# Kernel tuning notes

Hardware: AMD Instinct MI355X
Metric: run time of the kernel (lower is better)

## Reference

```python
import jax, jax.numpy as jnp
import numpy as np

N_NODES = 50000
N_EDGES = 800000
F_IN = 128
F_HID = 128
N_CLS = 1
E_TR = 100000
E_TE = 20000


def setup_inputs() -> dict:
    key = jax.random.key(0)
    ks = jax.random.split(key, 16)
    inp = {
        'x': jax.random.normal(ks[0], (N_NODES, F_IN), dtype=jnp.float32),
        'edge_index': jax.random.randint(ks[1], (2, N_EDGES), 0, N_NODES, dtype=jnp.int32),
        'pos_edges_train': jax.random.randint(ks[2], (2, E_TR), 0, N_NODES, dtype=jnp.int32),
        'neg_edges_train': jax.random.randint(ks[3], (2, E_TR), 0, N_NODES, dtype=jnp.int32),
        'pos_edges_test': jax.random.randint(ks[4], (2, E_TE), 0, N_NODES, dtype=jnp.int32),
        'neg_edges_test': jax.random.randint(ks[5], (2, E_TE), 0, N_NODES, dtype=jnp.int32),
    }
    s = 0.05
    inp['W0'] = jax.random.normal(ks[6], (F_IN, F_HID), dtype=jnp.float32) * s
    inp['b0'] = jnp.zeros((F_HID,), dtype=jnp.float32)
    inp['W1'] = jax.random.normal(ks[7], (F_HID, F_HID), dtype=jnp.float32) * s
    inp['b1'] = jnp.zeros((F_HID,), dtype=jnp.float32)
    inp['W2'] = jax.random.normal(ks[8], (F_HID, F_HID), dtype=jnp.float32) * s
    inp['b2'] = jnp.zeros((F_HID,), dtype=jnp.float32)
    inp['W3'] = jax.random.normal(ks[9], (F_HID, F_HID), dtype=jnp.float32) * s
    inp['b3'] = jnp.zeros((F_HID,), dtype=jnp.float32)
    inp['Wl1'] = jax.random.normal(ks[10], (2 * F_HID, F_HID), dtype=jnp.float32) * s
    inp['bl1'] = jnp.zeros((F_HID,), dtype=jnp.float32)
    inp['Wl2'] = jax.random.normal(ks[11], (F_HID, N_CLS), dtype=jnp.float32) * s
    inp['bl2'] = jnp.zeros((N_CLS,), dtype=jnp.float32)
    return inp


def _gcn_conv(h, W, b, src, dst, dis):
    # PyG GCNConv: out = D^{-1/2}(A+I)D^{-1/2} (h W) + b, with self loops folded in analytically
    hw = h @ W                                           # [N, F]
    msg = hw[src] * dis[src][:, None]                    # [E, F]
    agg = jax.ops.segment_sum(msg, dst, num_segments=N_NODES)
    return agg * dis[:, None] + hw * (dis ** 2)[:, None] + b


def _edge_feats(x, e):
    return jnp.concatenate([x[e[0]], x[e[1]]], axis=1)


def reference(x, edge_index, pos_edges_train, neg_edges_train, pos_edges_test, neg_edges_test,
              W0, b0, W1, b1, W2, b2, W3, b3, Wl1, bl1, Wl2, bl2):
    src, dst = edge_index[0], edge_index[1]
    # degree with self loop (+1), symmetric normalization
    deg = jax.ops.segment_sum(jnp.ones((src.shape[0],), jnp.float32), dst, num_segments=N_NODES) + 1.0
    dis = deg ** -0.5

    h = jax.nn.relu(_gcn_conv(x, W0, b0, src, dst, dis))
    h = jax.nn.relu(_gcn_conv(h, W1, b1, src, dst, dis))
    h = jax.nn.relu(_gcn_conv(h, W2, b2, src, dst, dis))
    h = _gcn_conv(h, W3, b3, src, dst, dis)

    x_train = jnp.concatenate([_edge_feats(h, pos_edges_train), _edge_feats(h, neg_edges_train)], axis=0)
    x_test = jnp.concatenate([_edge_feats(h, pos_edges_test), _edge_feats(h, neg_edges_test)], axis=0)
    n_train = x_train.shape[0]
    z = jnp.concatenate([x_train, x_test], axis=0)
    z = jax.nn.relu(z @ Wl1 + bl1)
    z = (z @ Wl2 + bl2).squeeze(1)
    return (z[:n_train], z[n_train:])
```

## Files before the change

kernel.cpp:

```cpp
#include <hip/hip_runtime.h>
#include <math.h>

#define NN 50000
#define NE 800000
#define FD 128
#define SCAN_B 196
#define NTR 100000
#define NTE 20000


__global__ __launch_bounds__(256) void k_zero_int(int* __restrict__ p, int n) {
    int i = blockIdx.x * 256 + threadIdx.x;
    if (i < n) p[i] = 0;
}

__global__ __launch_bounds__(256) void k_count(const int* __restrict__ dst, int* __restrict__ deg) {
    int e = blockIdx.x * 256 + threadIdx.x;
    if (e < NE) atomicAdd(&deg[dst[e]], 1);
}


__global__ __launch_bounds__(256) void k_scan1(const int* __restrict__ deg,
                                               int* __restrict__ partial,
                                               int* __restrict__ bsum,
                                               float* __restrict__ dis) {
    __shared__ int wsum[4];
    const int t = threadIdx.x, lane = t & 63, wid = t >> 6;
    const int i = blockIdx.x * 256 + t;
    int v = (i < NN) ? deg[i] : 0;
    int sc = v;
#pragma unroll
    for (int d = 1; d < 64; d <<= 1) {
        int o = __shfl_up(sc, d, 64);
        if (lane >= d) sc += o;
    }
    if (lane == 63) wsum[wid] = sc;
    __syncthreads();
    int pre = 0;
    for (int w = 0; w < wid; ++w) pre += wsum[w];
    if (i < NN) {
        partial[i] = pre + sc - v;
        dis[i] = (float)(1.0 / sqrt((double)(v + 1)));
    }
    if (t == 255) bsum[blockIdx.x] = pre + sc;
}

__global__ __launch_bounds__(256) void k_scan2(int* __restrict__ bsum) {
    __shared__ int wsum[4];
    const int t = threadIdx.x, lane = t & 63, wid = t >> 6;
    int v = (t < SCAN_B) ? bsum[t] : 0;
    int sc = v;
#pragma unroll
    for (int d = 1; d < 64; d <<= 1) {
        int o = __shfl_up(sc, d, 64);
        if (lane >= d) sc += o;
    }
    if (lane == 63) wsum[wid] = sc;
    __syncthreads();
    int pre = 0;
    for (int w = 0; w < wid; ++w) pre += wsum[w];
    if (t < SCAN_B) bsum[t] = pre + sc - v;
}

__global__ __launch_bounds__(256) void k_scan3(const int* __restrict__ partial,
                                               const int* __restrict__ bsum,
                                               int* __restrict__ offs,
                                               int* __restrict__ cursor) {
    const int i = blockIdx.x * 256 + threadIdx.x;
    if (i < NN) {
        int o = partial[i] + bsum[blockIdx.x];
        offs[i] = o;
        cursor[i] = o;
    }
    if (i == 0) offs[NN] = NE;
}


__global__ __launch_bounds__(256) void k_fill(const int* __restrict__ src, const int* __restrict__ dst,
                                              int* __restrict__ cursor, int* __restrict__ srcs_sorted) {
    int e = blockIdx.x * 256 + threadIdx.x;
    if (e < NE) {
        int d = dst[e];
        int p = atomicAdd(&cursor[d], 1);
        srcs_sorted[p] = src[e];
    }
}


__global__ __launch_bounds__(256) void k_gemm(const float* __restrict__ A,
                                              const float* __restrict__ W,
                                              const float* __restrict__ dis,
                                              float* __restrict__ C, int nrows) {
    __shared__ float As[64][128];
    const int t = threadIdx.x;
    const int row0 = blockIdx.x * 64;

    for (int idx = t; idx < 64 * 32; idx += 256) {
        int r = idx >> 5, c = idx & 31;
        float4 v = make_float4(0.f, 0.f, 0.f, 0.f);
        if (row0 + r < nrows)
            v = reinterpret_cast<const float4*>(A)[(size_t)(row0 + r) * 32 + c];
        reinterpret_cast<float4*>(&As[r][0])[c] = v;
    }
    __syncthreads();

    const int cg = t & 31;
    const int eg = t >> 5;
    float acc[8][4] = {{0.f}};

    const float4* W4 = reinterpret_cast<const float4*>(W);
    const float4* As4 = reinterpret_cast<const float4*>(As);

    for (int k4 = 0; k4 < 32; ++k4) {
        float4 w0 = W4[(k4 * 4 + 0) * 32 + cg];
        float4 w1 = W4[(k4 * 4 + 1) * 32 + cg];
        float4 w2 = W4[(k4 * 4 + 2) * 32 + cg];
        float4 w3 = W4[(k4 * 4 + 3) * 32 + cg];
#pragma unroll
        for (int i = 0; i < 8; ++i) {
            float4 a = As4[(eg * 8 + i) * 32 + k4];
            acc[i][0] += a.x * w0.x + a.y * w1.x + a.z * w2.x + a.w * w3.x;
            acc[i][1] += a.x * w0.y + a.y * w1.y + a.z * w2.y + a.w * w3.y;
            acc[i][2] += a.x * w0.z + a.y * w1.z + a.z * w2.z + a.w * w3.z;
            acc[i][3] += a.x * w0.w + a.y * w1.w + a.z * w2.w + a.w * w3.w;
        }
    }

#pragma unroll
    for (int i = 0; i < 8; ++i) {
        int r = row0 + eg * 8 + i;
        if (r < nrows) {
            float d = dis[r];
            float4 o = make_float4(acc[i][0] * d, acc[i][1] * d, acc[i][2] * d, acc[i][3] * d);
            reinterpret_cast<float4*>(C)[(size_t)r * 32 + cg] = o;
        }
    }
}


__global__ __launch_bounds__(256) void k_gemm_uv(const float* __restrict__ A,
                                                 const float* __restrict__ Wa,
                                                 const float* __restrict__ Wb,
                                                 float* __restrict__ U,
                                                 float* __restrict__ V, int nrows) {
    __shared__ float As[64][128];
    const int t = threadIdx.x;
    const int row0 = blockIdx.x * 64;

    for (int idx = t; idx < 64 * 32; idx += 256) {
        int r = idx >> 5, c = idx & 31;
        float4 v = make_float4(0.f, 0.f, 0.f, 0.f);
        if (row0 + r < nrows)
            v = reinterpret_cast<const float4*>(A)[(size_t)(row0 + r) * 32 + c];
        reinterpret_cast<float4*>(&As[r][0])[c] = v;
    }
    __syncthreads();

    const int cg = t & 31;
    const int eg = t >> 5;
    float accU[8][4] = {{0.f}};
    float accV[8][4] = {{0.f}};

    const float4* Wa4 = reinterpret_cast<const float4*>(Wa);
    const float4* Wb4 = reinterpret_cast<const float4*>(Wb);
    const float4* As4 = reinterpret_cast<const float4*>(As);

    for (int k = 0; k < 128; k += 2) {
        float4 wa0 = Wa4[(k + 0) * 32 + cg];
        float4 wa1 = Wa4[(k + 1) * 32 + cg];
        float4 wb0 = Wb4[(k + 0) * 32 + cg];
        float4 wb1 = Wb4[(k + 1) * 32 + cg];
#pragma unroll
        for (int i = 0; i < 8; ++i) {
            float2 a = reinterpret_cast<const float2*>(&As[eg * 8 + i][0])[k >> 1];
            accU[i][0] += a.x * wa0.x + a.y * wa1.x;
            accU[i][1] += a.x * wa0.y + a.y * wa1.y;
            accU[i][2] += a.x * wa0.z + a.y * wa1.z;
            accU[i][3] += a.x * wa0.w + a.y * wa1.w;
            accV[i][0] += a.x * wb0.x + a.y * wb1.x;
            accV[i][1] += a.x * wb0.y + a.y * wb1.y;
            accV[i][2] += a.x * wb0.z + a.y * wb1.z;
            accV[i][3] += a.x * wb0.w + a.y * wb1.w;
        }
    }

#pragma unroll
    for (int i = 0; i < 8; ++i) {
        int r = row0 + eg * 8 + i;
        if (r < nrows) {
            reinterpret_cast<float4*>(U)[(size_t)r * 32 + cg] =
                make_float4(accU[i][0], accU[i][1], accU[i][2], accU[i][3]);
            reinterpret_cast<float4*>(V)[(size_t)r * 32 + cg] =
                make_float4(accV[i][0], accV[i][1], accV[i][2], accV[i][3]);
        }
    }
}


template <bool RELU>
__global__ __launch_bounds__(256) void k_gather(const float* __restrict__ hws,
                                                const float* __restrict__ dis,
                                                const float* __restrict__ b,
                                                const int* __restrict__ offs,
                                                const int* __restrict__ srcs,
                                                float* __restrict__ out) {
    const int t = threadIdx.x;
    const int slice = blockIdx.x & 7;
    const int node = (blockIdx.x >> 3) * 64 + (t >> 2);
    if (node >= NN) return;
    const int f4 = slice * 4 + (t & 3);

    const float4* H4 = reinterpret_cast<const float4*>(hws);
    float4 acc = H4[(size_t)node * 32 + f4];
    const int e0 = offs[node], e1 = offs[node + 1];
    int e = e0;
    for (; e + 4 <= e1; e += 4) {
        int s0 = srcs[e + 0], s1 = srcs[e + 1], s2 = srcs[e + 2], s3 = srcs[e + 3];
        float4 v0 = H4[(size_t)s0 * 32 + f4];
        float4 v1 = H4[(size_t)s1 * 32 + f4];
        float4 v2 = H4[(size_t)s2 * 32 + f4];
        float4 v3 = H4[(size_t)s3 * 32 + f4];
        acc.x += v0.x + v1.x + v2.x + v3.x;
        acc.y += v0.y + v1.y + v2.y + v3.y;
        acc.z += v0.z + v1.z + v2.z + v3.z;
        acc.w += v0.w + v1.w + v2.w + v3.w;
    }
    for (; e < e1; ++e) {
        int s = srcs[e];
        float4 v = H4[(size_t)s * 32 + f4];
        acc.x += v.x; acc.y += v.y; acc.z += v.z; acc.w += v.w;
    }
    float d = dis[node];
    float4 bb = reinterpret_cast<const float4*>(b)[f4];
    float4 o;
    o.x = acc.x * d + bb.x;
    o.y = acc.y * d + bb.y;
    o.z = acc.z * d + bb.z;
    o.w = acc.w * d + bb.w;
    if (RELU) {
        o.x = fmaxf(o.x, 0.f); o.y = fmaxf(o.y, 0.f);
        o.z = fmaxf(o.z, 0.f); o.w = fmaxf(o.w, 0.f);
    }
    reinterpret_cast<float4*>(out)[(size_t)node * 32 + f4] = o;
}


__global__ __launch_bounds__(256) void k_edge_score(const float* __restrict__ U,
                                                    const float* __restrict__ V,
                                                    const int* __restrict__ tp,
                                                    const int* __restrict__ tn,
                                                    const int* __restrict__ sp,
                                                    const int* __restrict__ sn,
                                                    const float* __restrict__ bl1,
                                                    const float* __restrict__ Wl2,
                                                    const float* __restrict__ bl2,
                                                    float* __restrict__ out) {
    const int t = threadIdx.x;
    const int f4 = t & 31;
    const int e = blockIdx.x * 8 + (t >> 5);
    if (e >= 2 * NTR + 2 * NTE) return;

    int a, bn;
    if (e < NTR)                { a = tp[e];              bn = tp[e + NTR]; }
    else if (e < 2 * NTR)       { a = tn[e - NTR];        bn = tn[e]; }
    else if (e < 2 * NTR + NTE) { a = sp[e - 2 * NTR];    bn = sp[e - 2 * NTR + NTE]; }
    else                        { a = sn[e - 2 * NTR - NTE]; bn = sn[e - 2 * NTR]; }

    float4 u = reinterpret_cast<const float4*>(U)[(size_t)a * 32 + f4];
    float4 v = reinterpret_cast<const float4*>(V)[(size_t)bn * 32 + f4];
    float4 bb = reinterpret_cast<const float4*>(bl1)[f4];
    float4 w2 = reinterpret_cast<const float4*>(Wl2)[f4];

    float s = fmaxf(u.x + v.x + bb.x, 0.f) * w2.x
            + fmaxf(u.y + v.y + bb.y, 0.f) * w2.y
            + fmaxf(u.z + v.z + bb.z, 0.f) * w2.z
            + fmaxf(u.w + v.w + bb.w, 0.f) * w2.w;
#pragma unroll
    for (int m = 16; m >= 1; m >>= 1) s += __shfl_xor(s, m, 64);
    if (f4 == 0) out[e] = s + bl2[0];
}


extern "C" void kernel_launch(void* const* d_in, const int* in_sizes, int n_in,
                              void* d_out, int out_size, void* d_ws, size_t ws_size,
                              hipStream_t stream) {
    const float* x = (const float*)d_in[0];
    const int* ei = (const int*)d_in[1];
    const int* srcp = ei;
    const int* dstp = ei + NE;

    const int* e_tr_pos = (const int*)d_in[2];
    const int* e_tr_neg = (const int*)d_in[3];
    const int* e_te_pos = (const int*)d_in[4];
    const int* e_te_neg = (const int*)d_in[5];

    const float* W[4] = {(const float*)d_in[6], (const float*)d_in[8],
                         (const float*)d_in[10], (const float*)d_in[12]};
    const float* b[4] = {(const float*)d_in[7], (const float*)d_in[9],
                         (const float*)d_in[11], (const float*)d_in[13]};
    const float* Wl1 = (const float*)d_in[14];
    const float* bl1 = (const float*)d_in[15];
    const float* Wl2 = (const float*)d_in[16];
    const float* bl2 = (const float*)d_in[17];

    float* ws = (float*)d_ws;
    float* dis = ws;
    int* deg = (int*)(ws + 50176);
    int* offs = (int*)(ws + 100352);
    int* cursor = (int*)(ws + 150784);
    int* bsum = (int*)(ws + 200960);
    int* srcs = (int*)(ws + 201216);
    float* B0 = ws + 1001216;
    float* B1 = B0 + 6400000;
    float* B2 = B1 + 6400000;
    int* partial = (int*)B2;

    k_zero_int<<<(NN + 255) / 256, 256, 0, stream>>>(deg, NN);
    k_count<<<(NE + 255) / 256, 256, 0, stream>>>(dstp, deg);
    k_scan1<<<SCAN_B, 256, 0, stream>>>(deg, partial, bsum, dis);
    k_scan2<<<1, 256, 0, stream>>>(bsum);
    k_scan3<<<SCAN_B, 256, 0, stream>>>(partial, bsum, offs, cursor);
    k_fill<<<(NE + 255) / 256, 256, 0, stream>>>(srcp, dstp, cursor, srcs);

    const int gemm_blocks = (NN + 63) / 64;
    const int gath_blocks = ((NN + 63) / 64) * 8;

    float* hout[4] = {B1, B2, B1, B2};
    const float* hin = x;
    for (int l = 0; l < 4; ++l) {
        k_gemm<<<gemm_blocks, 256, 0, stream>>>(hin, W[l], dis, B0, NN);
        if (l < 3)
            k_gather<true><<<gath_blocks, 256, 0, stream>>>(B0, dis, b[l], offs, srcs, hout[l]);
        else
            k_gather<false><<<gath_blocks, 256, 0, stream>>>(B0, dis, b[l], offs, srcs, hout[l]);
        hin = hout[l];
    }

    const float* hfin = B2;
    float* Ubuf = B0;
    float* Vbuf = B1;
    k_gemm_uv<<<gemm_blocks, 256, 0, stream>>>(hfin, Wl1, Wl1 + 128 * 128, Ubuf, Vbuf, NN);

    float* out = (float*)d_out;
    const int n_all = 2 * NTR + 2 * NTE;
    k_edge_score<<<(n_all + 7) / 8, 256, 0, stream>>>(Ubuf, Vbuf,
                                                      e_tr_pos, e_tr_neg, e_te_pos, e_te_neg,
                                                      bl1, Wl2, bl2, out);
}
```

Before: 653.9 us.

## Remap gather to one node per 32 lanes, unroll by 8, prefetch GEMM weights

The gather kernel now assigns 32 lanes per node covering all 128 features in one block instead of splitting features into 8 block slices, so each neighbor row is read as one contiguous 512-byte access. Its edge loop is unrolled to 8 loads with a tree reduction to raise memory-level parallelism. The GEMM kernel software-prefetches the next weight slice into registers, and the UV GEMM switches to float4 LDS reads with a 4-wide k step. These changes target gather latency and load efficiency at the cost of more registers per thread.

```diff
diff --git a/kernel.cpp b/kernel.cpp
--- a/kernel.cpp
+++ b/kernel.cpp
@@ -111,11 +111,17 @@
     const float4* W4 = reinterpret_cast<const float4*>(W);
     const float4* As4 = reinterpret_cast<const float4*>(As);
 
+    float4 w0 = W4[0 * 32 + cg];
+    float4 w1 = W4[1 * 32 + cg];
+    float4 w2 = W4[2 * 32 + cg];
+    float4 w3 = W4[3 * 32 + cg];
+
     for (int k4 = 0; k4 < 32; ++k4) {
-        float4 w0 = W4[(k4 * 4 + 0) * 32 + cg];
-        float4 w1 = W4[(k4 * 4 + 1) * 32 + cg];
-        float4 w2 = W4[(k4 * 4 + 2) * 32 + cg];
-        float4 w3 = W4[(k4 * 4 + 3) * 32 + cg];
+        int kn = (k4 < 31) ? (k4 + 1) : 31;
+        float4 n0 = W4[(kn * 4 + 0) * 32 + cg];
+        float4 n1 = W4[(kn * 4 + 1) * 32 + cg];
+        float4 n2 = W4[(kn * 4 + 2) * 32 + cg];
+        float4 n3 = W4[(kn * 4 + 3) * 32 + cg];
 #pragma unroll
         for (int i = 0; i < 8; ++i) {
             float4 a = As4[(eg * 8 + i) * 32 + k4];
@@ -124,6 +130,7 @@
             acc[i][2] += a.x * w0.z + a.y * w1.z + a.z * w2.z + a.w * w3.z;
             acc[i][3] += a.x * w0.w + a.y * w1.w + a.z * w2.w + a.w * w3.w;
         }
+        w0 = n0; w1 = n1; w2 = n2; w3 = n3;
     }
 
 #pragma unroll
@@ -165,22 +172,26 @@
     const float4* Wb4 = reinterpret_cast<const float4*>(Wb);
     const float4* As4 = reinterpret_cast<const float4*>(As);
 
-    for (int k = 0; k < 128; k += 2) {
-        float4 wa0 = Wa4[(k + 0) * 32 + cg];
-        float4 wa1 = Wa4[(k + 1) * 32 + cg];
-        float4 wb0 = Wb4[(k + 0) * 32 + cg];
-        float4 wb1 = Wb4[(k + 1) * 32 + cg];
+    for (int k4 = 0; k4 < 32; ++k4) {
+        float4 wa0 = Wa4[(k4 * 4 + 0) * 32 + cg];
+        float4 wa1 = Wa4[(k4 * 4 + 1) * 32 + cg];
+        float4 wa2 = Wa4[(k4 * 4 + 2) * 32 + cg];
+        float4 wa3 = Wa4[(k4 * 4 + 3) * 32 + cg];
+        float4 wb0 = Wb4[(k4 * 4 + 0) * 32 + cg];
+        float4 wb1 = Wb4[(k4 * 4 + 1) * 32 + cg];
+        float4 wb2 = Wb4[(k4 * 4 + 2) * 32 + cg];
+        float4 wb3 = Wb4[(k4 * 4 + 3) * 32 + cg];
 #pragma unroll
         for (int i = 0; i < 8; ++i) {
-            float2 a = reinterpret_cast<const float2*>(&As[eg * 8 + i][0])[k >> 1];
-            accU[i][0] += a.x * wa0.x + a.y * wa1.x;
-            accU[i][1] += a.x * wa0.y + a.y * wa1.y;
-            accU[i][2] += a.x * wa0.z + a.y * wa1.z;
-            accU[i][3] += a.x * wa0.w + a.y * wa1.w;
-            accV[i][0] += a.x * wb0.x + a.y * wb1.x;
-            accV[i][1] += a.x * wb0.y + a.y * wb1.y;
-            accV[i][2] += a.x * wb0.z + a.y * wb1.z;
-            accV[i][3] += a.x * wb0.w + a.y * wb1.w;
+            float4 a = As4[(eg * 8 + i) * 32 + k4];
+            accU[i][0] += a.x * wa0.x + a.y * wa1.x + a.z * wa2.x + a.w * wa3.x;
+            accU[i][1] += a.x * wa0.y + a.y * wa1.y + a.z * wa2.y + a.w * wa3.y;
+            accU[i][2] += a.x * wa0.z + a.y * wa1.z + a.z * wa2.z + a.w * wa3.z;
+            accU[i][3] += a.x * wa0.w + a.y * wa1.w + a.z * wa2.w + a.w * wa3.w;
+            accV[i][0] += a.x * wb0.x + a.y * wb1.x + a.z * wb2.x + a.w * wb3.x;
+            accV[i][1] += a.x * wb0.y + a.y * wb1.y + a.z * wb2.y + a.w * wb3.y;
+            accV[i][2] += a.x * wb0.z + a.y * wb1.z + a.z * wb2.z + a.w * wb3.z;
+            accV[i][3] += a.x * wb0.w + a.y * wb1.w + a.z * wb2.w + a.w * wb3.w;
         }
     }
 
@@ -205,25 +216,29 @@
                                                 const int* __restrict__ srcs,
                                                 float* __restrict__ out) {
     const int t = threadIdx.x;
-    const int slice = blockIdx.x & 7;
-    const int node = (blockIdx.x >> 3) * 64 + (t >> 2);
+    const int f4 = t & 31;
+    const int node = blockIdx.x * 8 + (t >> 5);
     if (node >= NN) return;
-    const int f4 = slice * 4 + (t & 3);
 
     const float4* H4 = reinterpret_cast<const float4*>(hws);
     float4 acc = H4[(size_t)node * 32 + f4];
     const int e0 = offs[node], e1 = offs[node + 1];
     int e = e0;
-    for (; e + 4 <= e1; e += 4) {
+    for (; e + 8 <= e1; e += 8) {
         int s0 = srcs[e + 0], s1 = srcs[e + 1], s2 = srcs[e + 2], s3 = srcs[e + 3];
+        int s4 = srcs[e + 4], s5 = srcs[e + 5], s6 = srcs[e + 6], s7 = srcs[e + 7];
         float4 v0 = H4[(size_t)s0 * 32 + f4];
         float4 v1 = H4[(size_t)s1 * 32 + f4];
         float4 v2 = H4[(size_t)s2 * 32 + f4];
         float4 v3 = H4[(size_t)s3 * 32 + f4];
-        acc.x += v0.x + v1.x + v2.x + v3.x;
-        acc.y += v0.y + v1.y + v2.y + v3.y;
-        acc.z += v0.z + v1.z + v2.z + v3.z;
-        acc.w += v0.w + v1.w + v2.w + v3.w;
+        float4 v4 = H4[(size_t)s4 * 32 + f4];
+        float4 v5 = H4[(size_t)s5 * 32 + f4];
+        float4 v6 = H4[(size_t)s6 * 32 + f4];
+        float4 v7 = H4[(size_t)s7 * 32 + f4];
+        acc.x += ((v0.x + v1.x) + (v2.x + v3.x)) + ((v4.x + v5.x) + (v6.x + v7.x));
+        acc.y += ((v0.y + v1.y) + (v2.y + v3.y)) + ((v4.y + v5.y) + (v6.y + v7.y));
+        acc.z += ((v0.z + v1.z) + (v2.z + v3.z)) + ((v4.z + v5.z) + (v6.z + v7.z));
+        acc.w += ((v0.w + v1.w) + (v2.w + v3.w)) + ((v4.w + v5.w) + (v6.w + v7.w));
     }
     for (; e < e1; ++e) {
         int s = srcs[e];
@@ -323,7 +338,7 @@
     k_fill<<<(NE + 255) / 256, 256, 0, stream>>>(srcp, dstp, cursor, srcs);
 
     const int gemm_blocks = (NN + 63) / 64;
-    const int gath_blocks = ((NN + 63) / 64) * 8;
+    const int gath_blocks = (NN + 7) / 8;
 
     float* hout[4] = {B1, B2, B1, B2};
     const float* hin = x;
```

Result: faster. 581.1 us (-11.1%).
